# Optimization experiments

Hardware: AMD Instinct MI355X
Metric: run time of the kernel (lower is better)

The kernel has to match this reference:

```python
import jax, jax.numpy as jnp
import numpy as np

E = 8        # n_experts
H = 1024     # hidden
F = 1024     # ffn intermediate
K = 2        # top_k
B, T = 2, 1024


def setup_inputs() -> dict:
    key = jax.random.key(0)
    k1, k2, k3, k4 = jax.random.split(key, 4)
    return {
        "hidden_states": jax.random.normal(k1, (B, T, H), dtype=jnp.float32),
        "router_weight": jax.random.normal(k2, (E, H), dtype=jnp.float32),
        "gate_up_proj": jax.random.normal(k3, (E, 2 * F, H), dtype=jnp.float32),
        "down_proj": jax.random.normal(k4, (E, H, F), dtype=jnp.float32),
    }


def reference(hidden_states, router_weight, gate_up_proj, down_proj):
    b, t, h_dim = hidden_states.shape
    h = hidden_states.reshape(-1, h_dim)                      # [N, H]

    # Router: logits -> softmax -> top-k -> renormalize (matches FakeFusedRouter)
    logits = h @ router_weight.T                              # [N, E]
    probs = jax.nn.softmax(logits, axis=-1)
    top_v, top_i = jax.lax.top_k(probs, K)                    # [N, K]
    top_v = top_v / top_v.sum(axis=-1, keepdims=True)

    # Combine weights per expert: w[e, n] = sum_k top_v[n,k] * [top_i[n,k]==e]
    combine = (jax.nn.one_hot(top_i, E, dtype=top_v.dtype) * top_v[..., None]).sum(axis=1)  # [N, E]
    combine = combine.T                                       # [E, N]

    # Scan over experts: each expert runs its SwiGLU FFN over all tokens,
    # masked/weighted by combine (zero weight == token not routed there).
    def body(acc, xs):
        gu, dp, w = xs                                        # [2F,H], [H,F], [N]
        gate, up = jnp.split(h @ gu.T, 2, axis=-1)            # [N,F] each
        out = (jax.nn.silu(gate) * up) @ dp.T                 # [N,H]
        return acc + w[:, None] * out, None

    acc0 = jnp.zeros_like(h)
    final, _ = jax.lax.scan(body, acc0, (gate_up_proj, down_proj, combine))
    return final.reshape(b, t, h_dim)
```

## Files before the change

### kernel.cpp

```cpp
#include <hip/hip_runtime.h>


#define NTOK   2048
#define HDIM   1024
#define FDIM   1024
#define NEXP   8
#define NKROWS 4096
#define Q1LEN  256
#define Q2LEN  128

typedef __attribute__((ext_vector_type(8))) __bf16 bf16x8;
typedef __attribute__((ext_vector_type(4))) float  floatx4;

__device__ __forceinline__ unsigned short f2bf(float x) {
    unsigned int u = __builtin_bit_cast(unsigned int, x);
    u += 0x7FFFu + ((u >> 16) & 1u);
    return (unsigned short)(u >> 16);
}

__device__ __forceinline__ float bf2f(unsigned short v) {
    unsigned int u = (unsigned int)v << 16;
    return __builtin_bit_cast(float, u);
}

__device__ __forceinline__ uint4 pack8(float4 a, float4 b) {
    uint4 o;
    o.x = (unsigned)f2bf(a.x) | ((unsigned)f2bf(a.y) << 16);
    o.y = (unsigned)f2bf(a.z) | ((unsigned)f2bf(a.w) << 16);
    o.z = (unsigned)f2bf(b.x) | ((unsigned)f2bf(b.y) << 16);
    o.w = (unsigned)f2bf(b.z) | ((unsigned)f2bf(b.w) << 16);
    return o;
}

__device__ __forceinline__ void dma16(const void* g, void* l) {
    __builtin_amdgcn_global_load_lds(
        (const __attribute__((address_space(1))) unsigned int*)g,
        (__attribute__((address_space(3))) unsigned int*)l, 16, 0, 0);
}

__global__ __launch_bounds__(256) void k_pre(
    const float* __restrict__ gu, unsigned short* __restrict__ gubf,
    const float* __restrict__ dp, unsigned short* __restrict__ dpbf,
    const float* __restrict__ h, const float* __restrict__ rw,
    unsigned short* __restrict__ hbf,
    int* __restrict__ topk_idx, float* __restrict__ topk_w)
{
    const int b = blockIdx.x;
    if (b < 12288) {
        const float* src;
        unsigned short* dst;
        size_t base;
        if (b < 8192) { base = (size_t)b * 2048;          src = gu; dst = gubf; }
        else          { base = (size_t)(b - 8192) * 2048; src = dp; dst = dpbf; }
        size_t i = base + (size_t)threadIdx.x * 8;
        const float4* s = reinterpret_cast<const float4*>(src + i);
        float4 a = s[0], c = s[1];
        *reinterpret_cast<uint4*>(dst + i) = pack8(a, c);
        return;
    }
    const int lane = threadIdx.x & 63;
    const int wave = threadIdx.x >> 6;
    const int n = (b - 12288) * 4 + wave;

    const float4* hp = reinterpret_cast<const float4*>(h + (size_t)n * HDIM);
    uint2* hb = reinterpret_cast<uint2*>(hbf + (size_t)n * HDIM);
    float acc[NEXP];
#pragma unroll
    for (int e = 0; e < NEXP; ++e) acc[e] = 0.f;

#pragma unroll
    for (int i0 = 0; i0 < HDIM / 4; i0 += 64) {
        float4 hv = hp[i0 + lane];
        uint2 o;
        o.x = (unsigned)f2bf(hv.x) | ((unsigned)f2bf(hv.y) << 16);
        o.y = (unsigned)f2bf(hv.z) | ((unsigned)f2bf(hv.w) << 16);
        hb[i0 + lane] = o;
#pragma unroll
        for (int e = 0; e < NEXP; ++e) {
            float4 rv = reinterpret_cast<const float4*>(rw + e * HDIM)[i0 + lane];
            acc[e] += hv.x * rv.x + hv.y * rv.y + hv.z * rv.z + hv.w * rv.w;
        }
    }
#pragma unroll
    for (int e = 0; e < NEXP; ++e) {
#pragma unroll
        for (int off = 32; off > 0; off >>= 1)
            acc[e] += __shfl_xor(acc[e], off);
    }
    if (lane == 0) {
        int i0 = 0; float m0 = acc[0];
        for (int e = 1; e < NEXP; ++e) if (acc[e] > m0) { m0 = acc[e]; i0 = e; }
        int i1 = -1; float m1 = -3.0e38f;
        for (int e = 0; e < NEXP; ++e) if (e != i0 && acc[e] > m1) { m1 = acc[e]; i1 = e; }
        float d  = __expf(m1 - m0);
        float w0 = 1.f / (1.f + d);
        topk_idx[n * 2 + 0] = i0;
        topk_idx[n * 2 + 1] = i1;
        topk_w [n * 2 + 0] = w0;
        topk_w [n * 2 + 1] = 1.f - w0;
    }
}

__global__ __launch_bounds__(256) void k_build_perm(
    const int* __restrict__ topk_idx, const float* __restrict__ topk_w,
    int* __restrict__ offsets, int* __restrict__ perm_slot, float* __restrict__ row_w,
    int* __restrict__ q1, int* __restrict__ q2)
{
    __shared__ int cnt[NEXP];
    __shared__ int cur[NEXP];
    __shared__ int off[NEXP + 1];
    const int t = threadIdx.x;
    if (t < NEXP) cnt[t] = 0;
    __syncthreads();
    for (int s = t; s < NKROWS; s += 256) atomicAdd(&cnt[topk_idx[s]], 1);
    __syncthreads();
    if (t == 0) {
        int a = 0;
        for (int e = 0; e < NEXP; ++e) { off[e] = a; a += cnt[e]; cur[e] = off[e]; }
        off[NEXP] = a;
    }
    __syncthreads();
    for (int i = t; i < NEXP * Q1LEN; i += 256) {
        int e = i >> 8;
        int j = i & (Q1LEN - 1);
        int rts = (cnt[e] + 127) >> 7;
        int v = -1;
        if (j < 16 * rts) { int col = j / rts; int r = j - col * rts; v = e | (r << 4) | (col << 9); }
        q1[i] = v;
    }
    for (int i = t; i < NEXP * Q2LEN; i += 256) {
        int e = i >> 7;
        int j = i & (Q2LEN - 1);
        int rts = (cnt[e] + 127) >> 7;
        int v = -1;
        if (j < 8 * rts) { int col = j / rts; int r = j - col * rts; v = e | (r << 4) | (col << 9); }
        q2[i] = v;
    }
    for (int s = t; s < NKROWS; s += 256) {
        int e = topk_idx[s];
        int pos = atomicAdd(&cur[e], 1);
        perm_slot[pos] = s;
        row_w[pos] = topk_w[s];
    }
    if (t < NEXP + 1) offsets[t] = off[t];
}

__global__ __launch_bounds__(256, 2) void k_gemm1(
    const unsigned short* __restrict__ hbf, const unsigned short* __restrict__ gubf,
    const int* __restrict__ offsets, const int* __restrict__ perm_slot,
    const int* __restrict__ q1,
    unsigned short* __restrict__ act)
{
    const int bid = blockIdx.x;
    const int q = q1[(bid & 7) * Q1LEN + (bid >> 3)];
    if (q < 0) return;
    const int e  = q & 15;
    const int rt = (q >> 4) & 31;
    const int c0 = (q >> 9) * 64;
    const int off_e = offsets[e];
    const int n_e   = offsets[e + 1] - off_e;
    const int p0 = off_e + rt * 128;
    const int nr = min(128, n_e - rt * 128);

    __shared__ __align__(16) char smA [2][128 * 128];
    __shared__ __align__(16) char smBg[2][64 * 128];
    __shared__ __align__(16) char smBu[2][64 * 128];
    __shared__ int sTok[128];

    const int t = threadIdx.x;
    const int lane = t & 63;
    const int wv = t >> 6;
    const int wr = wv >> 1, wc = wv & 1;
    if (t < 128) sTok[t] = perm_slot[min(p0 + t, NKROWS - 1)] >> 1;
    __syncthreads();

    const int rin = lane >> 3;
    const int pre = ((lane & 7) << 4) ^ (rin << 4);

    const char* asrc[4];
    int aldo[4];
#pragma unroll
    for (int c = 0; c < 4; ++c) {
        int ch = wv * 4 + c;
        int row = ch * 8 + rin;
        asrc[c] = (const char*)(hbf + (size_t)sTok[row] * HDIM) + pre;
        aldo[c] = ch * 1024;
    }
    const unsigned short* guE = gubf + (size_t)e * (2 * FDIM) * HDIM;
    const char* gsrc[2];
    const char* usrc[2];
    int bldo[2];
#pragma unroll
    for (int c = 0; c < 2; ++c) {
        int ch = wv * 2 + c;
        int col = ch * 8 + rin;
        gsrc[c] = (const char*)(guE + (size_t)(c0 + col) * HDIM) + pre;
        usrc[c] = (const char*)(guE + (size_t)(FDIM + c0 + col) * HDIM) + pre;
        bldo[c] = ch * 1024;
    }

    floatx4 accg[4][2], accu[4][2];
#pragma unroll
    for (int m = 0; m < 4; ++m)
#pragma unroll
        for (int nn = 0; nn < 2; ++nn) { accg[m][nn] = (floatx4)0.f; accu[m][nn] = (floatx4)0.f; }

#define STAGE1(k0, buf)                                                         \
    {                                                                           \
        _Pragma("unroll")                                                       \
        for (int c = 0; c < 4; ++c) dma16(asrc[c] + (size_t)(k0) * 2, smA [buf] + aldo[c]); \
        _Pragma("unroll")                                                       \
        for (int c = 0; c < 2; ++c) dma16(gsrc[c] + (size_t)(k0) * 2, smBg[buf] + bldo[c]); \
        _Pragma("unroll")                                                       \
        for (int c = 0; c < 2; ++c) dma16(usrc[c] + (size_t)(k0) * 2, smBu[buf] + bldo[c]); \
    }

    STAGE1(0, 0);
    STAGE1(64, 1);

    for (int step = 0; step < 16; ++step) {
        if (step < 15) asm volatile("s_waitcnt vmcnt(8)" ::: "memory");
        else           asm volatile("s_waitcnt vmcnt(0)" ::: "memory");
        __builtin_amdgcn_s_barrier();
        __builtin_amdgcn_sched_barrier(0);
        const int cur = step & 1;
#pragma unroll
        for (int kk = 0; kk < 2; ++kk) {
            const int kA = kk * 64 + (lane >> 4) * 16;
            bf16x8 a[4], fg[2], fu[2];
#pragma unroll
            for (int m = 0; m < 4; ++m) {
                int row = wr * 64 + m * 16 + (lane & 15);
                a[m] = *reinterpret_cast<const bf16x8*>(&smA[cur][row * 128 + (kA ^ ((row & 7) << 4))]);
            }
#pragma unroll
            for (int nn = 0; nn < 2; ++nn) {
                int cc = wc * 32 + nn * 16 + (lane & 15);
                int ad = cc * 128 + (kA ^ ((cc & 7) << 4));
                fg[nn] = *reinterpret_cast<const bf16x8*>(&smBg[cur][ad]);
                fu[nn] = *reinterpret_cast<const bf16x8*>(&smBu[cur][ad]);
            }
#pragma unroll
            for (int m = 0; m < 4; ++m)
#pragma unroll
                for (int nn = 0; nn < 2; ++nn) {
                    accg[m][nn] = __builtin_amdgcn_mfma_f32_16x16x32_bf16(a[m], fg[nn], accg[m][nn], 0, 0, 0);
                    accu[m][nn] = __builtin_amdgcn_mfma_f32_16x16x32_bf16(a[m], fu[nn], accu[m][nn], 0, 0, 0);
                }
        }
        __builtin_amdgcn_sched_barrier(0);
        __builtin_amdgcn_s_barrier();
        if (step < 14) STAGE1((step + 2) * 64, cur);
    }
#undef STAGE1

#pragma unroll
    for (int m = 0; m < 4; ++m)
#pragma unroll
        for (int nn = 0; nn < 2; ++nn)
#pragma unroll
            for (int j = 0; j < 4; ++j) {
                int rr = wr * 64 + m * 16 + ((lane >> 4) << 2) + j;
                if (rr < nr) {
                    int f = c0 + wc * 32 + nn * 16 + (lane & 15);
                    float gg = accg[m][nn][j];
                    float uu = accu[m][nn][j];
                    float s = gg / (1.f + __expf(-gg));
                    act[(size_t)(p0 + rr) * FDIM + f] = f2bf(s * uu);
                }
            }
}

__global__ __launch_bounds__(256, 2) void k_gemm2(
    const unsigned short* __restrict__ act, const unsigned short* __restrict__ dpbf,
    const int* __restrict__ offsets, const int* __restrict__ perm_slot,
    const int* __restrict__ q2,
    const float* __restrict__ row_w, unsigned short* __restrict__ partial)
{
    const int bid = blockIdx.x;
    const int q = q2[(bid & 7) * Q2LEN + (bid >> 3)];
    if (q < 0) return;
    const int e  = q & 15;
    const int rt = (q >> 4) & 31;
    const int c0 = (q >> 9) * 128;
    const int off_e = offsets[e];
    const int n_e   = offsets[e + 1] - off_e;
    const int p0 = off_e + rt * 128;
    const int nr = min(128, n_e - rt * 128);

    __shared__ __align__(16) char smA[2][128 * 128];
    __shared__ __align__(16) char smB[2][128 * 128];
    __shared__ int   sSlot[128];
    __shared__ float sW[128];

    const int t = threadIdx.x;
    const int lane = t & 63;
    const int wv = t >> 6;
    const int wr = wv >> 1, wc = wv & 1;
    if (t < 128) {
        int p = min(p0 + t, NKROWS - 1);
        sSlot[t] = perm_slot[p];
        sW[t]    = row_w[p];
    }
    __syncthreads();

    const int rin = lane >> 3;
    const int pre = ((lane & 7) << 4) ^ (rin << 4);

    const char* asrc[4];
    int aldo[4];
#pragma unroll
    for (int c = 0; c < 4; ++c) {
        int ch = wv * 4 + c;
        int row = ch * 8 + rin;
        int p = min(p0 + row, NKROWS - 1);
        asrc[c] = (const char*)(act + (size_t)p * FDIM) + pre;
        aldo[c] = ch * 1024;
    }
    const unsigned short* dpE = dpbf + (size_t)e * HDIM * FDIM;
    const char* bsrc[4];
    int bldo[4];
#pragma unroll
    for (int c = 0; c < 4; ++c) {
        int ch = wv * 4 + c;
        int col = ch * 8 + rin;
        bsrc[c] = (const char*)(dpE + (size_t)(c0 + col) * FDIM) + pre;
        bldo[c] = ch * 1024;
    }

    floatx4 acc[4][4];
#pragma unroll
    for (int m = 0; m < 4; ++m)
#pragma unroll
        for (int nn = 0; nn < 4; ++nn) acc[m][nn] = (floatx4)0.f;

#define STAGE2(k0, buf)                                                         \
    {                                                                           \
        _Pragma("unroll")                                                       \
        for (int c = 0; c < 4; ++c) dma16(asrc[c] + (size_t)(k0) * 2, smA[buf] + aldo[c]); \
        _Pragma("unroll")                                                       \
        for (int c = 0; c < 4; ++c) dma16(bsrc[c] + (size_t)(k0) * 2, smB[buf] + bldo[c]); \
    }

    STAGE2(0, 0);
    STAGE2(64, 1);

    for (int step = 0; step < 16; ++step) {
        if (step < 15) asm volatile("s_waitcnt vmcnt(8)" ::: "memory");
        else           asm volatile("s_waitcnt vmcnt(0)" ::: "memory");
        __builtin_amdgcn_s_barrier();
        __builtin_amdgcn_sched_barrier(0);
        const int cur = step & 1;
#pragma unroll
        for (int kk = 0; kk < 2; ++kk) {
            const int kA = kk * 64 + (lane >> 4) * 16;
            bf16x8 a[4], fb[4];
#pragma unroll
            for (int m = 0; m < 4; ++m) {
                int row = wr * 64 + m * 16 + (lane & 15);
                a[m] = *reinterpret_cast<const bf16x8*>(&smA[cur][row * 128 + (kA ^ ((row & 7) << 4))]);
            }
#pragma unroll
            for (int nn = 0; nn < 4; ++nn) {
                int cc = wc * 64 + nn * 16 + (lane & 15);
                fb[nn] = *reinterpret_cast<const bf16x8*>(&smB[cur][cc * 128 + (kA ^ ((cc & 7) << 4))]);
            }
#pragma unroll
            for (int m = 0; m < 4; ++m)
#pragma unroll
                for (int nn = 0; nn < 4; ++nn)
                    acc[m][nn] = __builtin_amdgcn_mfma_f32_16x16x32_bf16(a[m], fb[nn], acc[m][nn], 0, 0, 0);
        }
        __builtin_amdgcn_sched_barrier(0);
        __builtin_amdgcn_s_barrier();
        if (step < 14) STAGE2((step + 2) * 64, cur);
    }
#undef STAGE2

#pragma unroll
    for (int m = 0; m < 4; ++m)
#pragma unroll
        for (int nn = 0; nn < 4; ++nn)
#pragma unroll
            for (int j = 0; j < 4; ++j) {
                int rr = wr * 64 + m * 16 + ((lane >> 4) << 2) + j;
                if (rr < nr) {
                    int hcol = c0 + wc * 64 + nn * 16 + (lane & 15);
                    partial[(size_t)sSlot[rr] * HDIM + hcol] = f2bf(sW[rr] * acc[m][nn][j]);
                }
            }
}

__global__ __launch_bounds__(256) void k_combine(
    const unsigned short* __restrict__ partial, float* __restrict__ out)
{
    int gid = blockIdx.x * 256 + threadIdx.x;
    int n = gid >> 7;
    int r = gid & 127;
    uint4 a = reinterpret_cast<const uint4*>(partial + (size_t)(2 * n) * HDIM)[r];
    uint4 b = reinterpret_cast<const uint4*>(partial + (size_t)(2 * n + 1) * HDIM)[r];
    float4 o0, o1;
    o0.x = bf2f(a.x & 0xFFFF) + bf2f(b.x & 0xFFFF);
    o0.y = bf2f(a.x >> 16)    + bf2f(b.x >> 16);
    o0.z = bf2f(a.y & 0xFFFF) + bf2f(b.y & 0xFFFF);
    o0.w = bf2f(a.y >> 16)    + bf2f(b.y >> 16);
    o1.x = bf2f(a.z & 0xFFFF) + bf2f(b.z & 0xFFFF);
    o1.y = bf2f(a.z >> 16)    + bf2f(b.z >> 16);
    o1.z = bf2f(a.w & 0xFFFF) + bf2f(b.w & 0xFFFF);
    o1.w = bf2f(a.w >> 16)    + bf2f(b.w >> 16);
    float4* op = reinterpret_cast<float4*>(out + (size_t)n * HDIM + r * 8);
    op[0] = o0;
    op[1] = o1;
}

extern "C" void kernel_launch(void* const* d_in, const int* in_sizes, int n_in,
                              void* d_out, int out_size, void* d_ws, size_t ws_size,
                              hipStream_t stream)
{
    const float* h  = (const float*)d_in[0];
    const float* rw = (const float*)d_in[1];
    const float* gu = (const float*)d_in[2];
    const float* dp = (const float*)d_in[3];
    float* out = (float*)d_out;

    char* ws = (char*)d_ws;
    int*            topk_idx  = (int*)   (ws + 0);
    float*          topk_w    = (float*) (ws + 16384);
    int*            offsets   = (int*)   (ws + 32768);
    int*            perm_slot = (int*)   (ws + 36864);
    float*          row_w     = (float*) (ws + 53248);
    int*            q1        = (int*)   (ws + 69632);
    int*            q2        = (int*)   (ws + 77824);
    unsigned short* hbf       = (unsigned short*)(ws + (1u  << 20));
    unsigned short* partial   = (unsigned short*)(ws + (1u  << 20));
    unsigned short* act       = (unsigned short*)(ws + (9u  << 20));
    unsigned short* gubf      = (unsigned short*)(ws + (17u << 20));
    unsigned short* dpbf      = (unsigned short*)(ws + (49u << 20));

    hipLaunchKernelGGL(k_pre,        dim3(12800),       dim3(256), 0, stream, gu, gubf, dp, dpbf, h, rw, hbf, topk_idx, topk_w);
    hipLaunchKernelGGL(k_build_perm, dim3(1),           dim3(256), 0, stream, topk_idx, topk_w, offsets, perm_slot, row_w, q1, q2);
    hipLaunchKernelGGL(k_gemm1,      dim3(8 * Q1LEN),   dim3(256), 0, stream, hbf, gubf, offsets, perm_slot, q1, act);
    hipLaunchKernelGGL(k_gemm2,      dim3(8 * Q2LEN),   dim3(256), 0, stream, act, dpbf, offsets, perm_slot, q2, row_w, partial);
    hipLaunchKernelGGL(k_combine,    dim3(1024),        dim3(256), 0, stream, partial, out);
}
```

Baseline: 107.6 us.

## Drop double-buffered GEMM pipeline for single buffer with higher occupancy; grid-stride weight conversion

Both expert GEMM kernels move from a two-stage double-buffered LDS pipeline with manual waitcnt/barrier scheduling to a single LDS buffer with load-sync-compute per k-step. The occupancy hint rises from 2 to 4 blocks per CU so other resident blocks can hide latency. The weight fp32-to-bf16 conversion in k_pre becomes a grid-stride loop over 2048 blocks instead of one block per chunk, cutting block launch overhead. The risk is that load latency inside each block is no longer overlapped with MFMA work and relies entirely on inter-block occupancy, plus extra barriers per step.

```diff
diff --git a/kernel.cpp b/kernel.cpp
--- a/kernel.cpp
+++ b/kernel.cpp
@@ -46,21 +46,23 @@
     int* __restrict__ topk_idx, float* __restrict__ topk_w)
 {
     const int b = blockIdx.x;
-    if (b < 12288) {
-        const float* src;
-        unsigned short* dst;
-        size_t base;
-        if (b < 8192) { base = (size_t)b * 2048;          src = gu; dst = gubf; }
-        else          { base = (size_t)(b - 8192) * 2048; src = dp; dst = dpbf; }
-        size_t i = base + (size_t)threadIdx.x * 8;
-        const float4* s = reinterpret_cast<const float4*>(src + i);
-        float4 a = s[0], c = s[1];
-        *reinterpret_cast<uint4*>(dst + i) = pack8(a, c);
+    if (b < 2048) {
+        for (int vb = b; vb < 12288; vb += 2048) {
+            const float* src;
+            unsigned short* dst;
+            size_t base;
+            if (vb < 8192) { base = (size_t)vb * 2048;          src = gu; dst = gubf; }
+            else           { base = (size_t)(vb - 8192) * 2048; src = dp; dst = dpbf; }
+            size_t i = base + (size_t)threadIdx.x * 8;
+            const float4* s = reinterpret_cast<const float4*>(src + i);
+            float4 a = s[0], c = s[1];
+            *reinterpret_cast<uint4*>(dst + i) = pack8(a, c);
+        }
         return;
     }
     const int lane = threadIdx.x & 63;
     const int wave = threadIdx.x >> 6;
-    const int n = (b - 12288) * 4 + wave;
+    const int n = (b - 2048) * 4 + wave;
 
     const float4* hp = reinterpret_cast<const float4*>(h + (size_t)n * HDIM);
     uint2* hb = reinterpret_cast<uint2*>(hbf + (size_t)n * HDIM);
@@ -145,7 +147,7 @@
     if (t < NEXP + 1) offsets[t] = off[t];
 }
 
-__global__ __launch_bounds__(256, 2) void k_gemm1(
+__global__ __launch_bounds__(256, 4) void k_gemm1(
     const unsigned short* __restrict__ hbf, const unsigned short* __restrict__ gubf,
     const int* __restrict__ offsets, const int* __restrict__ perm_slot,
     const int* __restrict__ q1,
@@ -162,9 +164,9 @@
     const int p0 = off_e + rt * 128;
     const int nr = min(128, n_e - rt * 128);
 
-    __shared__ __align__(16) char smA [2][128 * 128];
-    __shared__ __align__(16) char smBg[2][64 * 128];
-    __shared__ __align__(16) char smBu[2][64 * 128];
+    __shared__ __align__(16) char smA [128 * 128];
+    __shared__ __align__(16) char smBg[64 * 128];
+    __shared__ __align__(16) char smBu[64 * 128];
     __shared__ int sTok[128];
 
     const int t = threadIdx.x;
@@ -205,25 +207,15 @@
 #pragma unroll
         for (int nn = 0; nn < 2; ++nn) { accg[m][nn] = (floatx4)0.f; accu[m][nn] = (floatx4)0.f; }
 
-#define STAGE1(k0, buf)                                                         \
-    {                                                                           \
-        _Pragma("unroll")                                                       \
-        for (int c = 0; c < 4; ++c) dma16(asrc[c] + (size_t)(k0) * 2, smA [buf] + aldo[c]); \
-        _Pragma("unroll")                                                       \
-        for (int c = 0; c < 2; ++c) dma16(gsrc[c] + (size_t)(k0) * 2, smBg[buf] + bldo[c]); \
-        _Pragma("unroll")                                                       \
-        for (int c = 0; c < 2; ++c) dma16(usrc[c] + (size_t)(k0) * 2, smBu[buf] + bldo[c]); \
-    }
-
-    STAGE1(0, 0);
-    STAGE1(64, 1);
-
-    for (int step = 0; step < 16; ++step) {
-        if (step < 15) asm volatile("s_waitcnt vmcnt(8)" ::: "memory");
-        else           asm volatile("s_waitcnt vmcnt(0)" ::: "memory");
-        __builtin_amdgcn_s_barrier();
-        __builtin_amdgcn_sched_barrier(0);
-        const int cur = step & 1;
+    for (int k0 = 0; k0 < HDIM; k0 += 64) {
+        if (k0) __syncthreads();
+#pragma unroll
+        for (int c = 0; c < 4; ++c) dma16(asrc[c] + (size_t)k0 * 2, smA  + aldo[c]);
+#pragma unroll
+        for (int c = 0; c < 2; ++c) dma16(gsrc[c] + (size_t)k0 * 2, smBg + bldo[c]);
+#pragma unroll
+        for (int c = 0; c < 2; ++c) dma16(usrc[c] + (size_t)k0 * 2, smBu + bldo[c]);
+        __syncthreads();
 #pragma unroll
         for (int kk = 0; kk < 2; ++kk) {
             const int kA = kk * 64 + (lane >> 4) * 16;
@@ -231,14 +223,14 @@
 #pragma unroll
             for (int m = 0; m < 4; ++m) {
                 int row = wr * 64 + m * 16 + (lane & 15);
-                a[m] = *reinterpret_cast<const bf16x8*>(&smA[cur][row * 128 + (kA ^ ((row & 7) << 4))]);
+                a[m] = *reinterpret_cast<const bf16x8*>(smA + row * 128 + (kA ^ ((row & 7) << 4)));
             }
 #pragma unroll
             for (int nn = 0; nn < 2; ++nn) {
                 int cc = wc * 32 + nn * 16 + (lane & 15);
                 int ad = cc * 128 + (kA ^ ((cc & 7) << 4));
-                fg[nn] = *reinterpret_cast<const bf16x8*>(&smBg[cur][ad]);
-                fu[nn] = *reinterpret_cast<const bf16x8*>(&smBu[cur][ad]);
+                fg[nn] = *reinterpret_cast<const bf16x8*>(smBg + ad);
+                fu[nn] = *reinterpret_cast<const bf16x8*>(smBu + ad);
             }
 #pragma unroll
             for (int m = 0; m < 4; ++m)
@@ -248,11 +240,7 @@
                     accu[m][nn] = __builtin_amdgcn_mfma_f32_16x16x32_bf16(a[m], fu[nn], accu[m][nn], 0, 0, 0);
                 }
         }
-        __builtin_amdgcn_sched_barrier(0);
-        __builtin_amdgcn_s_barrier();
-        if (step < 14) STAGE1((step + 2) * 64, cur);
-    }
-#undef STAGE1
+    }
 
 #pragma unroll
     for (int m = 0; m < 4; ++m)
@@ -271,7 +259,7 @@
             }
 }
 
-__global__ __launch_bounds__(256, 2) void k_gemm2(
+__global__ __launch_bounds__(256, 4) void k_gemm2(
     const unsigned short* __restrict__ act, const unsigned short* __restrict__ dpbf,
     const int* __restrict__ offsets, const int* __restrict__ perm_slot,
     const int* __restrict__ q2,
@@ -288,8 +276,8 @@
     const int p0 = off_e + rt * 128;
     const int nr = min(128, n_e - rt * 128);
 
-    __shared__ __align__(16) char smA[2][128 * 128];
-    __shared__ __align__(16) char smB[2][128 * 128];
+    __shared__ __align__(16) char smA[128 * 128];
+    __shared__ __align__(16) char smB[128 * 128];
     __shared__ int   sSlot[128];
     __shared__ float sW[128];
 
@@ -334,23 +322,13 @@
 #pragma unroll
         for (int nn = 0; nn < 4; ++nn) acc[m][nn] = (floatx4)0.f;
 
-#define STAGE2(k0, buf)                                                         \
-    {                                                                           \
-        _Pragma("unroll")                                                       \
-        for (int c = 0; c < 4; ++c) dma16(asrc[c] + (size_t)(k0) * 2, smA[buf] + aldo[c]); \
-        _Pragma("unroll")                                                       \
-        for (int c = 0; c < 4; ++c) dma16(bsrc[c] + (size_t)(k0) * 2, smB[buf] + bldo[c]); \
-    }
-
-    STAGE2(0, 0);
-    STAGE2(64, 1);
-
-    for (int step = 0; step < 16; ++step) {
-        if (step < 15) asm volatile("s_waitcnt vmcnt(8)" ::: "memory");
-        else           asm volatile("s_waitcnt vmcnt(0)" ::: "memory");
-        __builtin_amdgcn_s_barrier();
-        __builtin_amdgcn_sched_barrier(0);
-        const int cur = step & 1;
+    for (int k0 = 0; k0 < FDIM; k0 += 64) {
+        if (k0) __syncthreads();
+#pragma unroll
+        for (int c = 0; c < 4; ++c) dma16(asrc[c] + (size_t)k0 * 2, smA + aldo[c]);
+#pragma unroll
+        for (int c = 0; c < 4; ++c) dma16(bsrc[c] + (size_t)k0 * 2, smB + bldo[c]);
+        __syncthreads();
 #pragma unroll
         for (int kk = 0; kk < 2; ++kk) {
             const int kA = kk * 64 + (lane >> 4) * 16;
@@ -358,12 +336,12 @@
 #pragma unroll
             for (int m = 0; m < 4; ++m) {
                 int row = wr * 64 + m * 16 + (lane & 15);
-                a[m] = *reinterpret_cast<const bf16x8*>(&smA[cur][row * 128 + (kA ^ ((row & 7) << 4))]);
+                a[m] = *reinterpret_cast<const bf16x8*>(smA + row * 128 + (kA ^ ((row & 7) << 4)));
             }
 #pragma unroll
             for (int nn = 0; nn < 4; ++nn) {
                 int cc = wc * 64 + nn * 16 + (lane & 15);
-                fb[nn] = *reinterpret_cast<const bf16x8*>(&smB[cur][cc * 128 + (kA ^ ((cc & 7) << 4))]);
+                fb[nn] = *reinterpret_cast<const bf16x8*>(smB + cc * 128 + (kA ^ ((cc & 7) << 4)));
             }
 #pragma unroll
             for (int m = 0; m < 4; ++m)
@@ -371,11 +349,7 @@
                 for (int nn = 0; nn < 4; ++nn)
                     acc[m][nn] = __builtin_amdgcn_mfma_f32_16x16x32_bf16(a[m], fb[nn], acc[m][nn], 0, 0, 0);
         }
-        __builtin_amdgcn_sched_barrier(0);
-        __builtin_amdgcn_s_barrier();
-        if (step < 14) STAGE2((step + 2) * 64, cur);
-    }
-#undef STAGE2
+    }
 
 #pragma unroll
     for (int m = 0; m < 4; ++m)
@@ -437,9 +411,9 @@
     unsigned short* gubf      = (unsigned short*)(ws + (17u << 20));
     unsigned short* dpbf      = (unsigned short*)(ws + (49u << 20));
 
-    hipLaunchKernelGGL(k_pre,        dim3(12800),       dim3(256), 0, stream, gu, gubf, dp, dpbf, h, rw, hbf, topk_idx, topk_w);
-    hipLaunchKernelGGL(k_build_perm, dim3(1),           dim3(256), 0, stream, topk_idx, topk_w, offsets, perm_slot, row_w, q1, q2);
-    hipLaunchKernelGGL(k_gemm1,      dim3(8 * Q1LEN),   dim3(256), 0, stream, hbf, gubf, offsets, perm_slot, q1, act);
-    hipLaunchKernelGGL(k_gemm2,      dim3(8 * Q2LEN),   dim3(256), 0, stream, act, dpbf, offsets, perm_slot, q2, row_w, partial);
-    hipLaunchKernelGGL(k_combine,    dim3(1024),        dim3(256), 0, stream, partial, out);
-}
+    hipLaunchKernelGGL(k_pre,        dim3(2560),      dim3(256), 0, stream, gu, gubf, dp, dpbf, h, rw, hbf, topk_idx, topk_w);
+    hipLaunchKernelGGL(k_build_perm, dim3(1),         dim3(256), 0, stream, topk_idx, topk_w, offsets, perm_slot, row_w, q1, q2);
+    hipLaunchKernelGGL(k_gemm1,      dim3(8 * Q1LEN), dim3(256), 0, stream, hbf, gubf, offsets, perm_slot, q1, act);
+    hipLaunchKernelGGL(k_gemm2,      dim3(8 * Q2LEN), dim3(256), 0, stream, act, dpbf, offsets, perm_slot, q2, row_w, partial);
+    hipLaunchKernelGGL(k_combine,    dim3(1024),      dim3(256), 0, stream, partial, out);
+}
```

Result: faster. 100.5 us (-6.6%).
